# Kernel tuning notes

Hardware: AMD Instinct MI355X
Metric: run time of the kernel (lower is better)

The kernel has to match this reference:

```python
import jax, jax.numpy as jnp
import numpy as np

NUM_HEADS = 16


def setup_inputs() -> dict:
    key = jax.random.key(0)
    ks = jax.random.split(key, 8)
    B, W, D = 128, 512, 2048
    s = 1.0 / np.sqrt(D)
    return {
        "x": jax.random.normal(ks[0], (B, D), jnp.float32),
        "buffer": jax.random.normal(ks[1], (B, W, D), jnp.float32),
        "Wq": jax.random.normal(ks[2], (D, D), jnp.float32) * s,
        "Wk": jax.random.normal(ks[3], (D, D), jnp.float32) * s,
        "Wv": jax.random.normal(ks[4], (D, D), jnp.float32) * s,
        "Wo": jax.random.normal(ks[5], (D, D), jnp.float32) * s,
        "Wg": jax.random.normal(ks[6], (D, 2 * D), jnp.float32) * (1.0 / np.sqrt(2 * D)),
        "bg": jnp.zeros((D,), jnp.float32),
    }


def reference(x, buffer, Wq, Wk, Wv, Wo, Wg, bg):
    B, D = x.shape
    H = NUM_HEADS
    Dh = D // H
    scale = Dh ** -0.5
    # steady-state ring buffer update: roll left, append x at last slot
    kv_seq = jnp.concatenate([buffer[:, 1:], x[:, None, :]], axis=1)  # [B, W, D]
    # projections (nn.Linear: y = x @ W.T)
    q = (x @ Wq.T).reshape(B, H, Dh)                      # [B, H, Dh]
    k = (kv_seq @ Wk.T).reshape(B, -1, H, Dh)             # [B, W, H, Dh]
    v = (kv_seq @ Wv.T).reshape(B, -1, H, Dh)
    # single-query attention over the window
    logits = jnp.einsum("bhd,bshd->bhs", q, k) * scale    # [B, H, W]
    attn = jax.nn.softmax(logits, axis=-1)
    out = jnp.einsum("bhs,bshd->bhd", attn, v).reshape(B, D)
    out = out @ Wo.T
    # gated residual
    g = jax.nn.sigmoid(jnp.concatenate([x, out], axis=-1) @ Wg.T + bg)
    return x + g * out
```

## Files before the change

### kernel.cpp

```cpp
#include <hip/hip_runtime.h>
#include <hip/hip_bf16.h>
#include <math.h>

#define B_   128
#define W_   512
#define D_   2048
#define H_   16
#define DH_  128

typedef __attribute__((ext_vector_type(4))) float f32x4;
typedef __attribute__((ext_vector_type(8))) short bf16x8;

typedef const __attribute__((address_space(1))) void* gvp;
typedef __attribute__((address_space(3))) void* lvp;

__device__ inline short f2bf(float f) {
  union { __hip_bfloat16 h; short s; } u;
  u.h = __float2bfloat16(f);
  return u.s;
}
__device__ inline float bf2f(unsigned short u) {
  return __uint_as_float(((unsigned)u) << 16);
}

#define LGKM_BARRIER() do {                                   \
    asm volatile("s_waitcnt lgkmcnt(0)" ::: "memory");        \
    __builtin_amdgcn_sched_barrier(0);                        \
    __builtin_amdgcn_s_barrier();                             \
    __builtin_amdgcn_sched_barrier(0);                        \
  } while (0)

template<bool BBF16>
__global__ __launch_bounds__(256) void gemm_mfma(
    const float* __restrict__ A, int a_rs, long a_hs,
    const float* __restrict__ A2, int a2_k,
    const void* __restrict__ Bv, int b_rs, long b_hs,
    float* __restrict__ C, int c_rs, long c_hs, long c_ks,
    int Kblk)
{
  __shared__ char sm[2][24576];

  const int t  = threadIdx.x;
  const int w  = t >> 6, l = t & 63, lo = l & 15, hi = l >> 4;
  const int wm = w >> 1, wn = w & 1;
  const int n0   = blockIdx.x * 64;
  const int head = blockIdx.y;
  const int ks   = blockIdx.z;
  const int kbeg = ks * Kblk;
  const int nit  = Kblk >> 6;

  const float* Ab;
  {
    const float* base = A;
    int koff = kbeg;
    if (A2 && kbeg >= a2_k) { base = A2; koff = kbeg - a2_k; }
    Ab = base + head * a_hs + koff;
  }
  const float*          Bf = (const float*)Bv          + (BBF16 ? 0 : head * b_hs + (long)n0 * b_rs + kbeg);
  const unsigned short* Bh = (const unsigned short*)Bv + (BBF16 ? head * b_hs + (long)n0 * b_rs + kbeg : 0);

  const int ar = t >> 2;
  const int ak = (t & 3) * 16;

  f32x4 acc[4][2] = {};

  auto load_tiles = [&](int it, float4* ar4, float4* br4) {
    const float* Ait = Ab + it * 64;
#pragma unroll
    for (int p = 0; p < 2; ++p) {
      const float* src = Ait + (long)(p * 64 + ar) * a_rs + ak;
#pragma unroll
      for (int qq = 0; qq < 4; ++qq) ar4[p * 4 + qq] = *(const float4*)(src + qq * 4);
    }
    if (BBF16) {
      const char* src = (const char*)(Bh + (long)ar * b_rs + it * 64 + ak);
      br4[0] = *(const float4*)(src);
      br4[1] = *(const float4*)(src + 16);
    } else {
      const float* src = Bf + (long)ar * b_rs + it * 64 + ak;
#pragma unroll
      for (int qq = 0; qq < 4; ++qq) br4[qq] = *(const float4*)(src + qq * 4);
    }
  };

  auto write_tiles = [&](int buf, const float4* ar4, const float4* br4) {
    char* As = sm[buf];
    char* Bs = sm[buf] + 16384;
#pragma unroll
    for (int p = 0; p < 2; ++p) {
      int m = p * 64 + ar;
      int base = m * 128 + ak * 2;
      int swz = (m & 7) << 4;
#pragma unroll
      for (int h2 = 0; h2 < 2; ++h2) {
        bf16x8 v;
        const float* f = (const float*)(ar4 + p * 4);
#pragma unroll
        for (int j = 0; j < 8; ++j) v[j] = f2bf(f[h2 * 8 + j]);
        *(bf16x8*)(As + ((base + h2 * 16) ^ swz)) = v;
      }
    }
    {
      int n = ar;
      int base = n * 128 + ak * 2;
      int swz = (n & 7) << 4;
      if (BBF16) {
#pragma unroll
        for (int h2 = 0; h2 < 2; ++h2)
          *(bf16x8*)(Bs + ((base + h2 * 16) ^ swz)) = ((const bf16x8*)br4)[h2];
      } else {
#pragma unroll
        for (int h2 = 0; h2 < 2; ++h2) {
          bf16x8 v;
          const float* f = (const float*)br4;
#pragma unroll
          for (int j = 0; j < 8; ++j) v[j] = f2bf(f[h2 * 8 + j]);
          *(bf16x8*)(Bs + ((base + h2 * 16) ^ swz)) = v;
        }
      }
    }
  };

  auto compute = [&](int buf) {
    const char* As = sm[buf];
    const char* Bs = sm[buf] + 16384;
#pragma unroll
    for (int kk = 0; kk < 2; ++kk) {
      bf16x8 af[4], bfr[2];
#pragma unroll
      for (int mi = 0; mi < 4; ++mi) {
        int m = wm * 64 + mi * 16 + lo;
        af[mi] = *(const bf16x8*)(As + ((m * 128 + (kk * 32 + hi * 8) * 2) ^ ((m & 7) << 4)));
      }
#pragma unroll
      for (int ni = 0; ni < 2; ++ni) {
        int n = wn * 32 + ni * 16 + lo;
        bfr[ni] = *(const bf16x8*)(Bs + ((n * 128 + (kk * 32 + hi * 8) * 2) ^ ((n & 7) << 4)));
      }
#pragma unroll
      for (int mi = 0; mi < 4; ++mi)
#pragma unroll
        for (int ni = 0; ni < 2; ++ni)
          acc[mi][ni] = __builtin_amdgcn_mfma_f32_16x16x32_bf16(af[mi], bfr[ni], acc[mi][ni], 0, 0, 0);
    }
  };

  float4 ar4[8], br4[4];
  load_tiles(0, ar4, br4);
  write_tiles(0, ar4, br4);
  __syncthreads();
  for (int it = 0; it < nit; ++it) {
    float4 na[8], nb[4];
    if (it + 1 < nit) load_tiles(it + 1, na, nb);
    compute(it & 1);
    if (it + 1 < nit) write_tiles((it + 1) & 1, na, nb);
    __syncthreads();
  }

  float* Cb = C + c_ks * ks + c_hs * head + n0;
#pragma unroll
  for (int mi = 0; mi < 4; ++mi)
#pragma unroll
    for (int ni = 0; ni < 2; ++ni)
#pragma unroll
      for (int r = 0; r < 4; ++r)
        Cb[(long)(wm * 64 + mi * 16 + hi * 4 + r) * c_rs + (wn * 32 + ni * 16 + lo)] = acc[mi][ni][r];
}

__global__ __launch_bounds__(256) void transpose_wk(
    const float* __restrict__ Wk, unsigned short* __restrict__ WkT)
{
  __shared__ float tile[64][68];
  const int t  = threadIdx.x;
  const int e0 = blockIdx.x * 64;
  const int d0 = blockIdx.y * 64;
  const int h  = blockIdx.z;
  {
    int d = t >> 2, eq = (t & 3) * 16;
    const float* src = Wk + (long)(h * DH_ + d0 + d) * D_ + e0 + eq;
#pragma unroll
    for (int qq = 0; qq < 4; ++qq)
      *(float4*)&tile[d][eq + qq * 4] = *(const float4*)(src + qq * 4);
  }
  __syncthreads();
  {
    int e = t >> 2, dq = (t & 3) * 16;
    unsigned short* dst = WkT + ((long)h * D_ + e0 + e) * DH_ + d0 + dq;
    bf16x8 v0, v1;
#pragma unroll
    for (int j = 0; j < 8; ++j) v0[j] = f2bf(tile[dq + j][e]);
#pragma unroll
    for (int j = 0; j < 8; ++j) v1[j] = f2bf(tile[dq + 8 + j][e]);
    *(bf16x8*)dst = v0;
    *(bf16x8*)(dst + 8) = v1;
  }
}

__global__ void reduce_add_k(const float* __restrict__ part, int ns, long stride,
                             long n, float* __restrict__ out)
{
  for (long i = (long)blockIdx.x * blockDim.x + threadIdx.x; i < n;
       i += (long)gridDim.x * blockDim.x) {
    float s = 0.f;
    for (int k = 0; k < ns; ++k) s += part[k * stride + i];
    out[i] = s;
  }
}

__global__ __launch_bounds__(1024, 4) void fused_attn(
    const float* __restrict__ x, const float* __restrict__ buffer,
    const float* __restrict__ qt, unsigned short* __restrict__ part,
    float* __restrict__ ml)
{
  __shared__ float kv[2 * 8 * 2048];
  __shared__ float lacc[16][8][16];
  __shared__ float pbuf[16][8];
  __shared__ float sbuf[16];

  const int b    = blockIdx.x;
  const int half = blockIdx.y;
  const int t    = threadIdx.x;
  const int w    = t >> 6;
  const int lane = t & 63;
  const int lo   = lane & 15;
  const int hi   = lane >> 4;
  const char* kvb = (const char*)kv;

  bf16x8 afrag[4];
  {
    const float* qrow = qt + ((long)b * H_ + lo) * D_;
    const float sc = 0.088388347648318447f;
#pragma unroll
    for (int kk = 0; kk < 4; ++kk) {
      int e0 = w * 128 + kk * 32 + hi * 8;
#pragma unroll
      for (int j = 0; j < 8; ++j) afrag[kk][j] = f2bf(qrow[e0 + j] * sc);
    }
  }

  float accE[16][2];
#pragma unroll
  for (int h = 0; h < 16; ++h) { accE[h][0] = 0.f; accE[h][1] = 0.f; }
  float m_run = -1e30f, l_run = 0.f;

  auto stage = [&](int sb, int tl) {
#pragma unroll
    for (int r = 0; r < 4; ++r) {
      int s = r * 2 + (w >> 3);
      int inrow = (w & 7) * 1024 + lane * 16;
      int srco = inrow ^ (s << 4);
      int s_glob = half * 256 + tl * 8 + s;
      const float* row = (s_glob < W_ - 1)
          ? buffer + (((long)(b * W_ + s_glob + 1)) << 11)
          : x + ((long)b << 11);
      __builtin_amdgcn_global_load_lds(
          (gvp)(row + (srco >> 2)),
          (lvp)(kv + sb * 16384 + r * 4096 + w * 256), 16, 0, 0);
    }
  };

  stage(0, 0);
  __syncthreads();

  for (int tile = 0; tile < 32; ++tile) {
    const int buf  = tile & 1;
    const int bufo = buf * 65536;

    if (tile + 1 < 32) stage(buf ^ 1, tile + 1);

    {
      f32x4 c4 = {0.f, 0.f, 0.f, 0.f};
      const int srow = lo & 7;
#pragma unroll
      for (int kk = 0; kk < 4; ++kk) {
        unsigned B0 = (unsigned)(srow * 8192 + (w * 128 + kk * 32 + hi * 8) * 4);
        unsigned o1 = B0 ^ (unsigned)(srow << 4);
        float4 f1 = *(const float4*)(kvb + bufo + o1);
        float4 f2 = *(const float4*)(kvb + bufo + (o1 ^ 16u));
        bf16x8 bf;
        bf[0] = f2bf(f1.x); bf[1] = f2bf(f1.y); bf[2] = f2bf(f1.z); bf[3] = f2bf(f1.w);
        bf[4] = f2bf(f2.x); bf[5] = f2bf(f2.y); bf[6] = f2bf(f2.z); bf[7] = f2bf(f2.w);
        c4 = __builtin_amdgcn_mfma_f32_16x16x32_bf16(afrag[kk], bf, c4, 0, 0, 0);
      }
      if (lo < 8) *(f32x4*)&lacc[w][lo][hi * 4] = c4;
    }
    LGKM_BARRIER();

    if (w < 4) {
      const int h = w * 4 + hi;
      const int s = lo & 7;
      float v = 0.f;
#pragma unroll
      for (int ww = 0; ww < 16; ++ww) v += lacc[ww][s][h];
      float mt = v;
      mt = fmaxf(mt, __shfl_xor(mt, 1));
      mt = fmaxf(mt, __shfl_xor(mt, 2));
      mt = fmaxf(mt, __shfl_xor(mt, 4));
      float m_new = fmaxf(m_run, mt);
      float scl = __expf(m_run - m_new);
      float p = __expf(v - m_new);
      float ps = p;
      ps += __shfl_xor(ps, 1);
      ps += __shfl_xor(ps, 2);
      ps += __shfl_xor(ps, 4);
      l_run = l_run * scl + ps;
      m_run = m_new;
      if (lo < 8) pbuf[h][s] = p;
      if (lo == 0) sbuf[h] = scl;
    }
    LGKM_BARRIER();

    const unsigned ebyte = (unsigned)((w * 128 + lane * 2) * 4);
    float2 kvp[8];
#pragma unroll
    for (int s = 0; s < 8; ++s) {
      unsigned Bx = (unsigned)(s * 8192) + ebyte;
      kvp[s] = *(const float2*)(kvb + bufo + (Bx ^ (unsigned)(s << 4)));
    }
#pragma unroll
    for (int h = 0; h < 16; ++h) {
      float scl = sbuf[h];
      float a0 = accE[h][0] * scl, a1 = accE[h][1] * scl;
      float4 pA = *(const float4*)&pbuf[h][0];
      float4 pB = *(const float4*)&pbuf[h][4];
      a0 += pA.x * kvp[0].x + pA.y * kvp[1].x + pA.z * kvp[2].x + pA.w * kvp[3].x
          + pB.x * kvp[4].x + pB.y * kvp[5].x + pB.z * kvp[6].x + pB.w * kvp[7].x;
      a1 += pA.x * kvp[0].y + pA.y * kvp[1].y + pA.z * kvp[2].y + pA.w * kvp[3].y
          + pB.x * kvp[4].y + pB.y * kvp[5].y + pB.z * kvp[6].y + pB.w * kvp[7].y;
      accE[h][0] = a0; accE[h][1] = a1;
    }
    __syncthreads();
  }

  {
    long base = ((long)half * B_ + b) * H_;
#pragma unroll
    for (int h = 0; h < 16; ++h) {
      long idx = (base + h) * D_ + w * 128 + lane * 2;
      unsigned u0 = (unsigned short)f2bf(accE[h][0]);
      unsigned u1 = (unsigned short)f2bf(accE[h][1]);
      *(unsigned*)(part + idx) = u0 | (u1 << 16);
    }
    if (w < 4 && lo == 0) {
      ml[(base + w * 4 + hi) * 2 + 0] = m_run;
      ml[(base + w * 4 + hi) * 2 + 1] = l_run;
    }
  }
}

__global__ __launch_bounds__(256) void combine_k(
    const unsigned short* __restrict__ part, const float* __restrict__ ml,
    float* __restrict__ vt)
{
  const int bh = blockIdx.x;
  const float m0 = ml[bh * 2],          l0 = ml[bh * 2 + 1];
  const float m1 = ml[(2048 + bh) * 2], l1 = ml[(2048 + bh) * 2 + 1];
  const float M  = fmaxf(m0, m1);
  const float w0 = __expf(m0 - M), w1 = __expf(m1 - M);
  const float inv = 1.0f / (w0 * l0 + w1 * l1);
  const unsigned short* p0 = part + (long)bh * D_;
  const unsigned short* p1 = part + (long)(2048 + bh) * D_;
  float* out = vt + (long)bh * D_;

  const int e = threadIdx.x * 8;
  ushort4 a1 = *(const ushort4*)(p0 + e);
  ushort4 a2 = *(const ushort4*)(p0 + e + 4);
  ushort4 b1 = *(const ushort4*)(p1 + e);
  ushort4 b2 = *(const ushort4*)(p1 + e + 4);
  float oa[8], ob[8];
  oa[0]=bf2f(a1.x); oa[1]=bf2f(a1.y); oa[2]=bf2f(a1.z); oa[3]=bf2f(a1.w);
  oa[4]=bf2f(a2.x); oa[5]=bf2f(a2.y); oa[6]=bf2f(a2.z); oa[7]=bf2f(a2.w);
  ob[0]=bf2f(b1.x); ob[1]=bf2f(b1.y); ob[2]=bf2f(b1.z); ob[3]=bf2f(b1.w);
  ob[4]=bf2f(b2.x); ob[5]=bf2f(b2.y); ob[6]=bf2f(b2.z); ob[7]=bf2f(b2.w);
#pragma unroll
  for (int j = 0; j < 8; ++j) out[e + j] = (w0 * oa[j] + w1 * ob[j]) * inv;
}

__global__ __launch_bounds__(256) void gate_final_k(
    const float* __restrict__ part, const float* __restrict__ bg,
    const float* __restrict__ x, const float* __restrict__ out1,
    float* __restrict__ y)
{
  const long i = (long)blockIdx.x * 256 + threadIdx.x;
  float z = bg[i & (D_ - 1)];
#pragma unroll
  for (int k = 0; k < 8; ++k) z += part[(long)k * (B_ * D_) + i];
  const float g = 1.0f / (1.0f + expf(-z));
  y[i] = x[i] + g * out1[i];
}

extern "C" void kernel_launch(void* const* d_in, const int* in_sizes, int n_in,
                              void* d_out, int out_size, void* d_ws, size_t ws_size,
                              hipStream_t stream)
{
  const float* x      = (const float*)d_in[0];
  const float* buffer = (const float*)d_in[1];
  const float* Wq     = (const float*)d_in[2];
  const float* Wk     = (const float*)d_in[3];
  const float* Wv     = (const float*)d_in[4];
  const float* Wo     = (const float*)d_in[5];
  const float* Wg     = (const float*)d_in[6];
  const float* bg     = (const float*)d_in[7];
  float* y = (float*)d_out;

  float* ws    = (float*)d_ws;
  float* q     = ws;
  float* qt    = ws + 262144;
  float* vt    = qt;
  unsigned short* part_a = (unsigned short*)(ws + 4456448);
  float* ml    = ws + 8650752;
  float* o0    = ws + 8658944;
  float* o1    = ws + 8921088;
  float* partg = ws + 9183232;
  unsigned short* wkT = (unsigned short*)(ws + 11280384);

  const long S = (long)B_ * D_;

  transpose_wk<<<dim3(32, 2, 16), 256, 0, stream>>>(Wk, wkT);

  gemm_mfma<false><<<dim3(32, 1, 8), 256, 0, stream>>>(
      x, D_, 0, nullptr, 1 << 30, Wq, D_, 0, partg, D_, 0, S, 256);
  reduce_add_k<<<512, 256, 0, stream>>>(partg, 8, S, S, q);

  gemm_mfma<true><<<dim3(32, 16, 1), 256, 0, stream>>>(
      q, D_, DH_, nullptr, 1 << 30, wkT, DH_, (long)D_ * DH_,
      qt, H_ * D_, D_, 0, DH_);

  fused_attn<<<dim3(B_, 2), 1024, 0, stream>>>(x, buffer, qt, part_a, ml);
  combine_k<<<B_ * H_, 256, 0, stream>>>(part_a, ml, vt);

  gemm_mfma<false><<<dim3(2, 16, 8), 256, 0, stream>>>(
      vt, H_ * D_, D_, nullptr, 1 << 30, Wv, D_, (long)DH_ * D_,
      partg, D_, DH_, S, 256);
  reduce_add_k<<<512, 256, 0, stream>>>(partg, 8, S, S, o0);

  gemm_mfma<false><<<dim3(32, 1, 8), 256, 0, stream>>>(
      o0, D_, 0, nullptr, 1 << 30, Wo, D_, 0, partg, D_, 0, S, 256);
  reduce_add_k<<<512, 256, 0, stream>>>(partg, 8, S, S, o1);

  gemm_mfma<false><<<dim3(32, 1, 8), 256, 0, stream>>>(
      x, D_, 0, o1, D_, Wg, 2 * D_, 0, partg, D_, 0, S, 512);
  gate_final_k<<<1024, 256, 0, stream>>>(partg, bg, x, o1, y);

  (void)in_sizes; (void)n_in; (void)out_size; (void)ws_size;
}
```

Measured before the change: 253.0 us.

## Stage KV tiles through registers as bf16 in a triple-buffered LDS ring

Replaces direct global-to-LDS fp32 loads with register-staged loads that are packed to bf16 (truncation via perm) before being written into a three-slot swizzled LDS ring, with loads issued two tiles ahead. This halves LDS footprint and LDS read traffic and removes per-tile fp32-to-bf16 conversion in the MFMA path, and lets the end-of-tile barrier drop to an LDS-count barrier. In exchange it adds register pressure for the staged float4s, uses truncation instead of rounding for the bf16 values (also used for the V accumulation now), and relies on the compiler to overlap the global loads with compute.

```diff
diff --git a/kernel.cpp b/kernel.cpp
--- a/kernel.cpp
+++ b/kernel.cpp
@@ -10,9 +10,6 @@
 
 typedef __attribute__((ext_vector_type(4))) float f32x4;
 typedef __attribute__((ext_vector_type(8))) short bf16x8;
-
-typedef const __attribute__((address_space(1))) void* gvp;
-typedef __attribute__((address_space(3))) void* lvp;
 
 __device__ inline short f2bf(float f) {
   union { __hip_bfloat16 h; short s; } u;
@@ -212,7 +209,7 @@
     const float* __restrict__ qt, unsigned short* __restrict__ part,
     float* __restrict__ ml)
 {
-  __shared__ float kv[2 * 8 * 2048];
+  __shared__ unsigned short kvh[3][8 * 2048];
   __shared__ float lacc[16][8][16];
   __shared__ float pbuf[16][8];
   __shared__ float sbuf[16];
@@ -221,10 +218,12 @@
   const int half = blockIdx.y;
   const int t    = threadIdx.x;
   const int w    = t >> 6;
-  const int lane = t & 63;
-  const int lo   = lane & 15;
-  const int hi   = lane >> 4;
-  const char* kvb = (const char*)kv;
+  const int ln   = t & 63;
+  const int lo   = ln & 15;
+  const int hi   = ln >> 4;
+
+  const int sr  = w >> 1;
+  const int shf = w & 1;
 
   bf16x8 afrag[4];
   {
@@ -243,44 +242,61 @@
   for (int h = 0; h < 16; ++h) { accE[h][0] = 0.f; accE[h][1] = 0.f; }
   float m_run = -1e30f, l_run = 0.f;
 
-  auto stage = [&](int sb, int tl) {
-#pragma unroll
-    for (int r = 0; r < 4; ++r) {
-      int s = r * 2 + (w >> 3);
-      int inrow = (w & 7) * 1024 + lane * 16;
-      int srco = inrow ^ (s << 4);
-      int s_glob = half * 256 + tl * 8 + s;
-      const float* row = (s_glob < W_ - 1)
-          ? buffer + (((long)(b * W_ + s_glob + 1)) << 11)
-          : x + ((long)b << 11);
-      __builtin_amdgcn_global_load_lds(
-          (gvp)(row + (srco >> 2)),
-          (lvp)(kv + sb * 16384 + r * 4096 + w * 256), 16, 0, 0);
+  float4 rg[4];
+
+  auto stage_load = [&](int tl) {
+    int s_glob = half * 256 + tl * 8 + sr;
+    const float* row = ((s_glob < W_ - 1)
+        ? buffer + (((long)(b * W_ + s_glob + 1)) << 11)
+        : x + ((long)b << 11)) + shf * 1024;
+#pragma unroll
+    for (int c = 0; c < 2; ++c) {
+      const float* p = row + c * 512 + ln * 8;
+      rg[c * 2]     = *(const float4*)p;
+      rg[c * 2 + 1] = *(const float4*)(p + 4);
     }
   };
 
-  stage(0, 0);
-  __syncthreads();
-
+  auto pack_write = [&](int bi) {
+    char* dst = (char*)kvh[bi] + sr * 4096 + shf * 2048;
+    const unsigned swz = (unsigned)((sr & 7) << 4);
+#pragma unroll
+    for (int c = 0; c < 2; ++c) {
+      unsigned u[4];
+      const float* f = (const float*)&rg[c * 2];
+#pragma unroll
+      for (int j = 0; j < 4; ++j)
+        u[j] = __builtin_amdgcn_perm(__float_as_uint(f[2 * j + 1]),
+                                     __float_as_uint(f[2 * j]), 0x07060302u);
+      *(uint4*)(dst + c * 1024 + (((unsigned)(ln * 16)) ^ swz)) = *(const uint4*)u;
+    }
+  };
+
+  stage_load(0);
+  pack_write(0);
+  stage_load(1);
+  LGKM_BARRIER();
+
+  int cur = 0;
   for (int tile = 0; tile < 32; ++tile) {
-    const int buf  = tile & 1;
-    const int bufo = buf * 65536;
-
-    if (tile + 1 < 32) stage(buf ^ 1, tile + 1);
+    const int nxt = (cur == 2) ? 0 : cur + 1;
+
+    if (tile + 1 < 32) pack_write(nxt);
+    if (tile + 2 < 32) stage_load(tile + 2);
+
+    const char* kb = (const char*)kvh[cur];
 
     {
       f32x4 c4 = {0.f, 0.f, 0.f, 0.f};
       const int srow = lo & 7;
+      const char* rowp = kb + srow * 4096;
+      const unsigned swz = (unsigned)(srow << 4);
 #pragma unroll
       for (int kk = 0; kk < 4; ++kk) {
-        unsigned B0 = (unsigned)(srow * 8192 + (w * 128 + kk * 32 + hi * 8) * 4);
-        unsigned o1 = B0 ^ (unsigned)(srow << 4);
-        float4 f1 = *(const float4*)(kvb + bufo + o1);
-        float4 f2 = *(const float4*)(kvb + bufo + (o1 ^ 16u));
-        bf16x8 bf;
-        bf[0] = f2bf(f1.x); bf[1] = f2bf(f1.y); bf[2] = f2bf(f1.z); bf[3] = f2bf(f1.w);
-        bf[4] = f2bf(f2.x); bf[5] = f2bf(f2.y); bf[6] = f2bf(f2.z); bf[7] = f2bf(f2.w);
-        c4 = __builtin_amdgcn_mfma_f32_16x16x32_bf16(afrag[kk], bf, c4, 0, 0, 0);
+        int e0 = w * 128 + kk * 32 + hi * 8;
+        unsigned byi = (unsigned)((e0 >> 9) * 1024) + ((((unsigned)((e0 >> 3) & 63)) * 16) ^ swz);
+        bf16x8 bv = *(const bf16x8*)(rowp + byi);
+        c4 = __builtin_amdgcn_mfma_f32_16x16x32_bf16(afrag[kk], bv, c4, 0, 0, 0);
       }
       if (lo < 8) *(f32x4*)&lacc[w][lo][hi * 4] = c4;
     }
@@ -310,33 +326,38 @@
     }
     LGKM_BARRIER();
 
-    const unsigned ebyte = (unsigned)((w * 128 + lane * 2) * 4);
-    float2 kvp[8];
-#pragma unroll
-    for (int s = 0; s < 8; ++s) {
-      unsigned Bx = (unsigned)(s * 8192) + ebyte;
-      kvp[s] = *(const float2*)(kvb + bufo + (Bx ^ (unsigned)(s << 4)));
-    }
-#pragma unroll
-    for (int h = 0; h < 16; ++h) {
-      float scl = sbuf[h];
-      float a0 = accE[h][0] * scl, a1 = accE[h][1] * scl;
-      float4 pA = *(const float4*)&pbuf[h][0];
-      float4 pB = *(const float4*)&pbuf[h][4];
-      a0 += pA.x * kvp[0].x + pA.y * kvp[1].x + pA.z * kvp[2].x + pA.w * kvp[3].x
-          + pB.x * kvp[4].x + pB.y * kvp[5].x + pB.z * kvp[6].x + pB.w * kvp[7].x;
-      a1 += pA.x * kvp[0].y + pA.y * kvp[1].y + pA.z * kvp[2].y + pA.w * kvp[3].y
-          + pB.x * kvp[4].y + pB.y * kvp[5].y + pB.z * kvp[6].y + pB.w * kvp[7].y;
-      accE[h][0] = a0; accE[h][1] = a1;
-    }
-    __syncthreads();
+    {
+      const int e0 = w * 128 + ln * 2;
+      const unsigned base = (unsigned)((e0 >> 9) * 1024 + (((e0 >> 3) & 63) * 16) + (e0 & 7) * 2);
+      float ke0[8], ke1[8];
+#pragma unroll
+      for (int s = 0; s < 8; ++s) {
+        unsigned u = *(const unsigned*)(kb + s * 4096 + (base ^ ((unsigned)(s << 4))));
+        ke0[s] = __uint_as_float(u << 16);
+        ke1[s] = __uint_as_float(u & 0xffff0000u);
+      }
+#pragma unroll
+      for (int h = 0; h < 16; ++h) {
+        float scl = sbuf[h];
+        float a0 = accE[h][0] * scl, a1 = accE[h][1] * scl;
+        float4 pA = *(const float4*)&pbuf[h][0];
+        float4 pB = *(const float4*)&pbuf[h][4];
+        a0 += pA.x * ke0[0] + pA.y * ke0[1] + pA.z * ke0[2] + pA.w * ke0[3]
+            + pB.x * ke0[4] + pB.y * ke0[5] + pB.z * ke0[6] + pB.w * ke0[7];
+        a1 += pA.x * ke1[0] + pA.y * ke1[1] + pA.z * ke1[2] + pA.w * ke1[3]
+            + pB.x * ke1[4] + pB.y * ke1[5] + pB.z * ke1[6] + pB.w * ke1[7];
+        accE[h][0] = a0; accE[h][1] = a1;
+      }
+    }
+    LGKM_BARRIER();
+    cur = nxt;
   }
 
   {
     long base = ((long)half * B_ + b) * H_;
 #pragma unroll
     for (int h = 0; h < 16; ++h) {
-      long idx = (base + h) * D_ + w * 128 + lane * 2;
+      long idx = (base + h) * D_ + w * 128 + ln * 2;
       unsigned u0 = (unsigned short)f2bf(accE[h][0]);
       unsigned u1 = (unsigned short)f2bf(accE[h][1]);
       *(unsigned*)(part + idx) = u0 | (u1 << 16);
```

After: 327.6 us. +29.5%, slower.
